# Performance work log

Measured on AMD Instinct MI355X. Metric: run time of the kernel, lower is better.

Reference implementation:

```python
import jax, jax.numpy as jnp
import numpy as np

H, D, H1, L = 4, 128, 512, 2
EPS = 1e-5


def _seg_softmax(logits, seg, n):
    # numerically stable softmax over edges grouped by destination node
    mx = jax.ops.segment_max(logits, seg, num_segments=n)
    mx = jnp.where(jnp.isfinite(mx), mx, 0.0)
    e = jnp.exp(logits - mx[seg])
    s = jax.ops.segment_sum(e, seg, num_segments=n)
    return e / (s[seg] + 1e-16)


def _layernorm(x, g, b):
    mu = x.mean(-1, keepdims=True)
    var = ((x - mu) ** 2).mean(-1, keepdims=True)
    return (x - mu) * jax.lax.rsqrt(var + EPS) * g + b


def _hgt_forward(x_paper, x_author, Wp_paper, bp_paper, Wp_author, bp_author,
                 Wk, bk, Wq, bq, Wv, bv, Wa, ba, skip,
                 a_rel, m_rel, p_rel, ln_g, ln_b,
                 W256, b256, W128, b128,
                 ei_cites, ei_writes, ei_writtenby):
    Np, Na = x_paper.shape[0], x_author.shape[0]
    hp = x_paper @ Wp_paper + bp_paper   # [Np, 512]
    ha = x_author @ Wp_author + bp_author  # [Na, 512]
    scale = 1.0 / jnp.sqrt(jnp.float32(D))

    def kqv(h, l, t):
        k = (h @ Wk[l, t] + bk[l, t]).reshape(-1, H, D)
        q = (h @ Wq[l, t] + bq[l, t]).reshape(-1, H, D)
        v = (h @ Wv[l, t] + bv[l, t]).reshape(-1, H, D)
        return k, q, v

    def rel_msgs(k_src, v_src, q_dst, ei, l, r):
        src, dst = ei[0], ei[1]
        kr = jnp.einsum('nhd,hde->nhe', k_src, a_rel[l, r])  # per-src-node relation transform
        vr = jnp.einsum('nhd,hde->nhe', v_src, m_rel[l, r])
        alpha = (q_dst[dst] * kr[src]).sum(-1) * p_rel[l, r] * scale  # [E, H]
        return alpha, vr[src], dst

    for l in range(L):
        kp, qp, vp = kqv(hp, l, 0)
        ka, qa, va = kqv(ha, l, 1)
        # paper receives: cites (paper->paper, rel 0) + writes (author->paper, rel 1)
        a0, m0, d0 = rel_msgs(kp, vp, qp, ei_cites, l, 0)
        a1, m1, d1 = rel_msgs(ka, va, qp, ei_writes, l, 1)
        al = jnp.concatenate([a0, a1], 0)
        mg = jnp.concatenate([m0, m1], 0)
        ds = jnp.concatenate([d0, d1], 0)
        al = _seg_softmax(al, ds, Np)
        op = jax.ops.segment_sum(al[:, :, None] * mg, ds, num_segments=Np).reshape(Np, H1)
        # author receives: written_by (paper->author, rel 2)
        a2, m2, d2 = rel_msgs(kp, vp, qa, ei_writtenby, l, 2)
        a2 = _seg_softmax(a2, d2, Na)
        oa = jax.ops.segment_sum(a2[:, :, None] * m2, d2, num_segments=Na).reshape(Na, H1)
        # per-dst-type output linear on gelu, then sigmoid-gated skip (HGTConv)
        op = jax.nn.gelu(op, approximate=False) @ Wa[l, 0] + ba[l, 0]
        oa = jax.nn.gelu(oa, approximate=False) @ Wa[l, 1] + ba[l, 1]
        sp = jax.nn.sigmoid(skip[l, 0])
        sa = jax.nn.sigmoid(skip[l, 1])
        op = sp * op + (1.0 - sp) * hp
        oa = sa * oa + (1.0 - sa) * ha
        # encoder wrapper: residual + shared LayerNorm + ReLU (dropout = identity in eval)
        hp = jax.nn.relu(_layernorm(op + hp, ln_g[l], ln_b[l]))
        ha = jax.nn.relu(_layernorm(oa + ha, ln_g[l], ln_b[l]))

    hp = jax.nn.relu(hp @ W256 + b256) @ W128 + b128
    ha = jax.nn.relu(ha @ W256 + b256) @ W128 + b128
    return hp, ha


def setup_inputs() -> dict:
    key = jax.random.key(0)
    ks = iter(jax.random.split(key, 48))
    Np, Na, IN = 30000, 10000, 768
    Ec, Ew, Eb = 150000, 80000, 80000
    f = lambda *s: jax.random.normal(next(ks), s, jnp.float32) * 0.02
    ri = lambda n, e: jax.random.randint(next(ks), (e,), 0, n, jnp.int32)
    inp = {
        'x_paper': jax.random.normal(next(ks), (Np, IN), jnp.float32),
        'x_author': jax.random.normal(next(ks), (Na, IN), jnp.float32),
        'Wp_paper': f(IN, H1), 'bp_paper': jnp.zeros((H1,), jnp.float32),
        'Wp_author': f(IN, H1), 'bp_author': jnp.zeros((H1,), jnp.float32),
        'Wk': f(L, 2, H1, H1), 'bk': jnp.zeros((L, 2, H1), jnp.float32),
        'Wq': f(L, 2, H1, H1), 'bq': jnp.zeros((L, 2, H1), jnp.float32),
        'Wv': f(L, 2, H1, H1), 'bv': jnp.zeros((L, 2, H1), jnp.float32),
        'Wa': f(L, 2, H1, H1), 'ba': jnp.zeros((L, 2, H1), jnp.float32),
        'skip': jnp.ones((L, 2), jnp.float32),
        'a_rel': f(L, 3, H, D, D), 'm_rel': f(L, 3, H, D, D),
        'p_rel': jnp.ones((L, 3, H), jnp.float32),
        'ln_g': jnp.ones((L, H1), jnp.float32), 'ln_b': jnp.zeros((L, H1), jnp.float32),
        'W256': f(H1, 256), 'b256': jnp.zeros((256,), jnp.float32),
        'W128': f(256, 128), 'b128': jnp.zeros((128,), jnp.float32),
        'ei_cites': jnp.stack([ri(Np, Ec), ri(Np, Ec)]),
        'ei_writes': jnp.stack([ri(Na, Ew), ri(Np, Ew)]),
        'ei_writtenby': jnp.stack([ri(Np, Eb), ri(Na, Eb)]),
    }
    return inp


def reference(x_paper, x_author, Wp_paper, bp_paper, Wp_author, bp_author,
              Wk, bk, Wq, bq, Wv, bv, Wa, ba, skip,
              a_rel, m_rel, p_rel, ln_g, ln_b,
              W256, b256, W128, b128,
              ei_cites, ei_writes, ei_writtenby):
    return _hgt_forward(x_paper, x_author, Wp_paper, bp_paper, Wp_author, bp_author,
                        Wk, bk, Wq, bq, Wv, bv, Wa, ba, skip,
                        a_rel, m_rel, p_rel, ln_g, ln_b,
                        W256, b256, W128, b128,
                        ei_cites, ei_writes, ei_writtenby)
```

## Files before the change

### kernel.cpp

```cpp
#include <hip/hip_runtime.h>
#include <hip/hip_bf16.h>
#include <math.h>

#define NHEAD 4
#define DH 128
#define HID 512
#define NLAY 2
#define NP 30000
#define NA 10000
#define INDIM 768
#define EC 150000
#define EW 80000
#define EB 80000
#define NQP 2560
#define NQA 1536

typedef __hip_bfloat16 bf16;
typedef __attribute__((ext_vector_type(8))) short bf16x8;
typedef __attribute__((ext_vector_type(4))) float f32x4;
typedef __attribute__((ext_vector_type(4))) unsigned int u32x4;

__device__ __forceinline__ unsigned short f2bu(float f){ bf16 t = __float2bfloat16(f); return *(unsigned short*)&t; }
__device__ __forceinline__ float bu2f(unsigned short u){ return __uint_as_float((unsigned)u << 16); }

__device__ __forceinline__ void load8b(const bf16* __restrict__ p, int i8, float* o){
  uint4 r = ((const uint4*)p)[i8];
  o[0]=__uint_as_float(r.x<<16); o[1]=__uint_as_float(r.x&0xffff0000u);
  o[2]=__uint_as_float(r.y<<16); o[3]=__uint_as_float(r.y&0xffff0000u);
  o[4]=__uint_as_float(r.z<<16); o[5]=__uint_as_float(r.z&0xffff0000u);
  o[6]=__uint_as_float(r.w<<16); o[7]=__uint_as_float(r.w&0xffff0000u);
}

__device__ __forceinline__ void gload16(const void* g, void* l) {
  __builtin_amdgcn_global_load_lds((const __attribute__((address_space(1))) void*)g,
                                   (__attribute__((address_space(3))) void*)l, 16, 0, 0);
}

struct GemmPair {
  const bf16 *A0, *A1, *B0, *B1;
  const float *b0, *b1;
  void *C0, *C1;
  int lda0, lda1, ldb0, ldb1, ldc0, ldc1;
  int M0, M1, K0, K1;
  int act0, act1, bf0, bf1;
  int nbn0, nbn1, nw0;
};

#define TSTRIDE 132

__global__ __launch_bounds__(256)
void mfma_gemm2(GemmPair gp)
{
  __shared__ __align__(16) short smem[32768];
  const int tid = threadIdx.x;
  const int lane = tid & 63, w = tid >> 6;
  const int nwg = gridDim.x;
  const int bid = blockIdx.x;
  const int xcd = bid & 7, pos = bid >> 3;
  const int q8 = nwg >> 3, r8 = nwg & 7;
  const int work = (xcd < r8 ? xcd * (q8 + 1) : r8 * (q8 + 1) + (xcd - r8) * q8) + pos;
  const int g = work >= gp.nw0;
  const int w2 = g ? work - gp.nw0 : work;
  const bf16* A  = g ? gp.A1 : gp.A0;
  const bf16* Bt = g ? gp.B1 : gp.B0;
  const float* bias = g ? gp.b1 : gp.b0;
  void* Cv = g ? gp.C1 : gp.C0;
  const int lda = g ? gp.lda1 : gp.lda0;
  const int ldb = g ? gp.ldb1 : gp.ldb0;
  const int ldc = g ? gp.ldc1 : gp.ldc0;
  const int M = g ? gp.M1 : gp.M0;
  const int K = g ? gp.K1 : gp.K0;
  const int act = g ? gp.act1 : gp.act0;
  const int isbf = g ? gp.bf1 : gp.bf0;
  const int nbn = g ? gp.nbn1 : gp.nbn0;
  const int brow = (w2 / nbn) * 128, bcol = (w2 % nbn) * 128;
  const int wr = w >> 1, wc = w & 1;

  f32x4 acc[4][4];
#pragma unroll
  for (int m = 0; m < 4; m++)
#pragma unroll
    for (int n = 0; n < 4; n++) acc[m][n] = (f32x4){0.f, 0.f, 0.f, 0.f};

  auto STAGE = [&](int buf, int k0) {
    short* Asb = smem + buf * 8192;
    short* Bsb = smem + 16384 + buf * 8192;
#pragma unroll
    for (int i = 0; i < 4; i++) {
      int chunk = i * 4 + w;
      int c_lin = chunk * 64 + lane;
      int row = c_lin >> 3;
      int kc = ((c_lin & 7) ^ (row & 7)) * 8;
      int growA = brow + row; growA = growA < M ? growA : M - 1;
      gload16(A + (size_t)growA * lda + k0 + kc, Asb + chunk * 512);
      gload16(Bt + (size_t)(bcol + row) * ldb + k0 + kc, Bsb + chunk * 512);
    }
  };

  const int nk = K >> 6;
  STAGE(0, 0);
  __syncthreads();
  int buf = 0;
  for (int t = 0; t < nk; t++) {
    if (t + 1 < nk) STAGE(buf ^ 1, (t + 1) << 6);
    const short* Asb = smem + buf * 8192;
    const short* Bsb = smem + 16384 + buf * 8192;
#pragma unroll
    for (int kk = 0; kk < 2; kk++) {
      const int ke = kk * 32 + (lane >> 4) * 8;
      bf16x8 af[4], bq[4];
#pragma unroll
      for (int m = 0; m < 4; m++) {
        int row = wr * 64 + m * 16 + (lane & 15);
        af[m] = *(const bf16x8*)(Asb + row * 64 + (ke ^ ((row & 7) << 3)));
      }
#pragma unroll
      for (int n = 0; n < 4; n++) {
        int col = wc * 64 + n * 16 + (lane & 15);
        bq[n] = *(const bf16x8*)(Bsb + col * 64 + (ke ^ ((col & 7) << 3)));
      }
#pragma unroll
      for (int m = 0; m < 4; m++)
#pragma unroll
        for (int n = 0; n < 4; n++)
          acc[m][n] = __builtin_amdgcn_mfma_f32_16x16x32_bf16(af[m], bq[n], acc[m][n], 0, 0, 0);
    }
    __syncthreads();
    buf ^= 1;
  }

  if (isbf) {
#pragma unroll
    for (int m = 0; m < 4; m++) {
      int row0 = wr * 64 + m * 16 + (lane >> 4) * 4;
#pragma unroll
      for (int n = 0; n < 4; n++) {
        int col = wc * 64 + n * 16 + (lane & 15);
        float bv = bias ? bias[bcol + col] : 0.f;
#pragma unroll
        for (int r = 0; r < 4; r++) {
          float v = acc[m][n][r] + bv;
          if (act) v = fmaxf(v, 0.f);
          smem[(row0 + r) * TSTRIDE + col] = (short)f2bu(v);
        }
      }
    }
    __syncthreads();
#pragma unroll
    for (int it = 0; it < 8; it++) {
      int chunk = it * 256 + tid;
      int row = chunk >> 4, c16 = chunk & 15;
      int gr = brow + row;
      if (gr < M) {
        u32x4 v = *(const u32x4*)(smem + row * TSTRIDE + c16 * 8);
        __builtin_nontemporal_store(v,
            (u32x4*)((unsigned short*)Cv + (size_t)gr * ldc + bcol + c16 * 8));
      }
    }
  } else {
#pragma unroll
    for (int m = 0; m < 4; m++) {
      int gr0 = brow + wr * 64 + m * 16 + (lane >> 4) * 4;
#pragma unroll
      for (int n = 0; n < 4; n++) {
        int gc = bcol + wc * 64 + n * 16 + (lane & 15);
        float bv = bias ? bias[gc] : 0.f;
#pragma unroll
        for (int r = 0; r < 4; r++) {
          int gr = gr0 + r;
          if (gr < M) {
            float v = acc[m][n][r] + bv;
            if (act) v = fmaxf(v, 0.f);
            __builtin_nontemporal_store(v, (float*)Cv + (size_t)gr * ldc + gc);
          }
        }
      }
    }
  }
}

struct FuseArgs {
  const float* W[12];
  const float* rel[12];
  const float* bin[12];
  float* out[12];
  float* bout[12];
};
struct TrArgs {
  const float* src[20];
  bf16* dst[20];
};
struct CopyB { const float* src[4]; float* dst[4]; };

__global__ __launch_bounds__(256)
void gemm_fuse(FuseArgs fa)
{
  int c = blockIdx.z >> 2, h = blockIdx.z & 3;
  const float* A = fa.W[c] + h * 128;
  const float* B = fa.rel[c] + (size_t)h * 128 * 128;
  float* C = fa.out[c] + h * 128;
  __shared__ float Ast[64][17];
  __shared__ float Bst[16][64];
  const int tid = threadIdx.x;
  const int tx = tid & 15, ty = tid >> 4;
  const int bm = blockIdx.x * 64, bn = blockIdx.y * 64;
  float acc[4][4] = {};
  for (int k0 = 0; k0 < 128; k0 += 16) {
#pragma unroll
    for (int i = 0; i < 4; i++) {
      int lin = tid + i * 256;
      int m = lin >> 4, kk = lin & 15;
      Ast[m][kk] = A[(size_t)(bm + m) * 512 + k0 + kk];
      int kb = lin >> 6, nb = lin & 63;
      Bst[kb][nb] = B[(size_t)(k0 + kb) * 128 + bn + nb];
    }
    __syncthreads();
#pragma unroll
    for (int kk = 0; kk < 16; kk++) {
      float a[4], b[4];
#pragma unroll
      for (int i = 0; i < 4; i++) a[i] = Ast[ty * 4 + i][kk];
#pragma unroll
      for (int j = 0; j < 4; j++) b[j] = Bst[kk][tx * 4 + j];
#pragma unroll
      for (int i = 0; i < 4; i++)
#pragma unroll
        for (int j = 0; j < 4; j++)
          acc[i][j] = fmaf(a[i], b[j], acc[i][j]);
    }
    __syncthreads();
  }
#pragma unroll
  for (int i = 0; i < 4; i++)
#pragma unroll
    for (int j = 0; j < 4; j++)
      C[(size_t)(bm + ty * 4 + i) * 512 + bn + tx * 4 + j] = acc[i][j];
}

__global__ __launch_bounds__(256)
void transpose20(TrArgs ta)
{
  int c = blockIdx.z;
  const float* in = ta.src[c];
  bf16* o = ta.dst[c];
  __shared__ float t[32][33];
  int bn = blockIdx.x * 32, bk = blockIdx.y * 32;
  int x = threadIdx.x, y = threadIdx.y;
#pragma unroll
  for (int i = 0; i < 32; i += 8)
    t[y + i][x] = in[(size_t)(bk + y + i) * 512 + bn + x];
  __syncthreads();
#pragma unroll
  for (int i = 0; i < 32; i += 8)
    o[(size_t)(bn + y + i) * 512 + bk + x] = __float2bfloat16(t[x][y + i]);
}

__global__ __launch_bounds__(512)
void bias_fuse_all(FuseArgs fa)
{
  int c = blockIdx.x;
  int j = threadIdx.x;
  int h = j >> 7, e = j & 127;
  const float* bh = fa.bin[c] + h * DH;
  const float* rh = fa.rel[c] + (size_t)h * DH * DH;
  float s = 0.f;
  for (int d = 0; d < DH; d++) s = fmaf(bh[d], rh[d * DH + e], s);
  fa.bout[c][j] = s;
}

__global__ __launch_bounds__(512)
void copy_bias(CopyB cb)
{
  cb.dst[blockIdx.x][threadIdx.x] = cb.src[blockIdx.x][threadIdx.x];
}

__global__ __launch_bounds__(256)
void transpose_to_bf16(const float* __restrict__ in, bf16* __restrict__ out,
                       int K_, int N_)
{
  __shared__ float t[32][33];
  int bn = blockIdx.x * 32, bk = blockIdx.y * 32;
  int x = threadIdx.x, y = threadIdx.y;
#pragma unroll
  for (int i = 0; i < 32; i += 8) {
    int k = bk + y + i, n = bn + x;
    if (k < K_ && n < N_) t[y + i][x] = in[(size_t)k * N_ + n];
  }
  __syncthreads();
#pragma unroll
  for (int i = 0; i < 32; i += 8) {
    int n = bn + y + i, k = bk + x;
    if (n < N_ && k < K_) out[(size_t)n * K_ + k] = __float2bfloat16(t[x][y + i]);
  }
}

__global__ __launch_bounds__(256)
void f32_to_bf16_2(const float* __restrict__ s0, bf16* __restrict__ d0, long long n0,
                   const float* __restrict__ s1, bf16* __restrict__ d1, long long n1)
{
  long long i = ((long long)blockIdx.x * 256 + threadIdx.x) * 4;
  const float* s; bf16* d;
  if (i < n0) { s = s0; d = d0; }
  else { i -= n0; if (i >= n1) return; s = s1; d = d1; }
  float4 v = *(const float4*)(s + i);
  ushort4 o;
  o.x = f2bu(v.x); o.y = f2bu(v.y); o.z = f2bu(v.z); o.w = f2bu(v.w);
  *(ushort4*)(d + i) = o;
}

__global__ __launch_bounds__(256)
void build_hist(const int* __restrict__ ei_dst, int E, int* __restrict__ deg)
{
  int i = blockIdx.x * 256 + threadIdx.x;
  if (i < E) atomicAdd(&deg[ei_dst[i]], 1);
}

__global__ __launch_bounds__(256)
void scan_blk(const int* __restrict__ deg, int n, int* __restrict__ rowptr,
              int* __restrict__ bsum)
{
  __shared__ int sh[256];
  int t = threadIdx.x;
  int base = blockIdx.x * 1024 + t * 4;
  int v0 = 0, v1 = 0, v2 = 0, v3 = 0;
  if (base + 3 < n) {
    int4 v = *(const int4*)(deg + base);
    v0 = v.x; v1 = v.y; v2 = v.z; v3 = v.w;
  } else {
    if (base < n)     v0 = deg[base];
    if (base + 1 < n) v1 = deg[base + 1];
    if (base + 2 < n) v2 = deg[base + 2];
    if (base + 3 < n) v3 = deg[base + 3];
  }
  int s = v0 + v1 + v2 + v3;
  sh[t] = s;
  __syncthreads();
#pragma unroll
  for (int off = 1; off < 256; off <<= 1) {
    int tv = (t >= off) ? sh[t - off] : 0;
    __syncthreads();
    sh[t] += tv;
    __syncthreads();
  }
  int excl = sh[t] - s;
  if (t == 255) bsum[blockIdx.x] = sh[255];
  if (base < n)     rowptr[base] = excl;
  if (base + 1 < n) rowptr[base + 1] = excl + v0;
  if (base + 2 < n) rowptr[base + 2] = excl + v0 + v1;
  if (base + 3 < n) rowptr[base + 3] = excl + v0 + v1 + v2;
}

__global__ __launch_bounds__(64)
void scan_bsum(int* __restrict__ bsum, int nb, int* __restrict__ rowptr_end)
{
  int t = threadIdx.x;
  int v = (t < nb) ? bsum[t] : 0;
  int inc = v;
#pragma unroll
  for (int off = 1; off < 64; off <<= 1) {
    int o = __shfl_up(inc, off);
    if (t >= off) inc += o;
  }
  if (t < nb) bsum[t] = inc - v;
  if (t == nb - 1) *rowptr_end = inc;
}

__global__ __launch_bounds__(256)
void scan_add(int* __restrict__ rowptr, const int* __restrict__ bsum, int n)
{
  int add = bsum[blockIdx.x];
  if (add == 0) return;
  int i = blockIdx.x * 1024 + threadIdx.x * 4;
  if (i < n)     rowptr[i] += add;
  if (i + 1 < n) rowptr[i + 1] += add;
  if (i + 2 < n) rowptr[i + 2] += add;
  if (i + 3 < n) rowptr[i + 3] += add;
}

__global__ __launch_bounds__(256)
void build_scatter(const int* __restrict__ ei, int E, int flag,
                   const int* __restrict__ rowptr, int* __restrict__ cursor,
                   int* __restrict__ srcs)
{
  int e = blockIdx.x * 256 + threadIdx.x;
  if (e >= E) return;
  int src = ei[e];
  int dst = ei[E + e];
  int pos = rowptr[dst] + atomicAdd(&cursor[dst], 1);
  srcs[pos] = src | flag;
}

__global__ __launch_bounds__(256)
void csr_attn_agg2(const int* __restrict__ rowptrP, const int* __restrict__ srcsP,
                   const int* __restrict__ rowptrA, const int* __restrict__ srcsA,
                   const bf16* __restrict__ qkvP, const bf16* __restrict__ qkvA,
                   const float* __restrict__ prl, float scale,
                   bf16* __restrict__ agP, bf16* __restrict__ agA)
{
  int node = blockIdx.x * 4 + (threadIdx.x >> 6);
  int lane = threadIdx.x & 63;
  int h = lane >> 4;
  const int* rp; const int* srcs;
  const bf16* q; const bf16 *t0, *t1;
  int ld0, off0, ld1, off1;
  float p0, p1;
  bf16* outp;
  if (node < NP) {
    rp = rowptrP; srcs = srcsP;
    q = qkvP + (size_t)node * NQP;
    t0 = qkvP; ld0 = NQP; off0 = 512;
    t1 = qkvA; ld1 = NQA; off1 = 512;
    p0 = prl[h] * scale; p1 = prl[4 + h] * scale;
    outp = agP + (size_t)node * HID;
  } else {
    int r = node - NP;
    if (r >= NA) return;
    rp = rowptrA; srcs = srcsA; node = r;
    q = qkvA + (size_t)r * NQA;
    t0 = qkvP; ld0 = NQP; off0 = 1536;
    t1 = qkvP; ld1 = NQP; off1 = 1536;
    p0 = prl[8 + h] * scale; p1 = p0;
    outp = agA + (size_t)r * HID;
  }
  float qv[8];
  load8b(q, lane, qv);
  int beg = rp[node], end = rp[node + 1];
  float m = -INFINITY, s = 0.f;
  float acc[8] = {};
  for (int p = beg; p < end; ++p) {
    int se = srcs[p];
    int src = se & 0x3FFFFFFF;
    bool f1 = (se & 0x40000000) != 0;
    const bf16* row = f1 ? (t1 + (size_t)src * ld1 + off1)
                         : (t0 + (size_t)src * ld0 + off0);
    float kv[8], vv[8];
    load8b(row, lane, kv);
    load8b(row + 512, lane, vv);
    float a = 0.f;
#pragma unroll
    for (int i = 0; i < 8; i++) a = fmaf(qv[i], kv[i], a);
    a += __shfl_xor(a, 1);
    a += __shfl_xor(a, 2);
    a += __shfl_xor(a, 4);
    a += __shfl_xor(a, 8);
    a *= f1 ? p1 : p0;
    if (a > m + 8.f) {
      float sc = __expf(m - a);
      s *= sc;
#pragma unroll
      for (int i = 0; i < 8; i++) acc[i] *= sc;
      m = a;
    }
    float wgt = __expf(a - m);
    s += wgt;
#pragma unroll
    for (int i = 0; i < 8; i++) acc[i] = fmaf(wgt, vv[i], acc[i]);
  }
  float inv = 1.f / (s + 1e-16f);
  unsigned short gg[8];
#pragma unroll
  for (int i = 0; i < 8; i++) {
    float v = acc[i] * inv;
    gg[i] = f2bu(0.5f * v * (1.f + erff(v * 0.70710678118654752f)));
  }
  uint4 o;
  o.x = gg[0] | ((unsigned)gg[1] << 16);
  o.y = gg[2] | ((unsigned)gg[3] << 16);
  o.z = gg[4] | ((unsigned)gg[5] << 16);
  o.w = gg[6] | ((unsigned)gg[7] << 16);
  *(uint4*)(outp + lane * 8) = o;
}

__global__ __launch_bounds__(256)
void skip_ln_relu2(const bf16* __restrict__ oplP, const bf16* __restrict__ oplA,
                   bf16* __restrict__ hP, bf16* __restrict__ hA,
                   const float* __restrict__ skip2,
                   const float* __restrict__ g, const float* __restrict__ b)
{
  int row = blockIdx.x;
  const bf16* orow; bf16* hrow; float sk;
  if (row < NP) {
    orow = oplP + (size_t)row * HID; hrow = hP + (size_t)row * HID; sk = skip2[0];
  } else {
    int r = row - NP;
    orow = oplA + (size_t)r * HID; hrow = hA + (size_t)r * HID; sk = skip2[1];
  }
  float sp = 1.f / (1.f + expf(-sk));
  int t = threadIdx.x;
  ushort2 ov = ((const ushort2*)orow)[t];
  ushort2 hv = ((ushort2*)hrow)[t];
  float t0 = sp * bu2f(ov.x) + (2.f - sp) * bu2f(hv.x);
  float t1 = sp * bu2f(ov.y) + (2.f - sp) * bu2f(hv.y);
  float s = t0 + t1, ss = t0 * t0 + t1 * t1;
#pragma unroll
  for (int off = 32; off; off >>= 1) {
    s += __shfl_down(s, off);
    ss += __shfl_down(ss, off);
  }
  __shared__ float sh[8];
  int wid = t >> 6, lane = t & 63;
  if (lane == 0) { sh[wid] = s; sh[4 + wid] = ss; }
  __syncthreads();
  if (t == 0) {
    float S = 0, SS = 0;
    for (int wv = 0; wv < 4; wv++) { S += sh[wv]; SS += sh[4 + wv]; }
    sh[0] = S; sh[4] = SS;
  }
  __syncthreads();
  float mu = sh[0] * (1.f / 512.f);
  float var = sh[4] * (1.f / 512.f) - mu * mu;
  float inv = rsqrtf(var + 1e-5f);
  float y0 = (t0 - mu) * inv * g[2 * t] + b[2 * t];
  float y1 = (t1 - mu) * inv * g[2 * t + 1] + b[2 * t + 1];
  ushort2 o;
  o.x = f2bu(fmaxf(y0, 0.f));
  o.y = f2bu(fmaxf(y1, 0.f));
  ((ushort2*)hrow)[t] = o;
}

static inline void mgemm2(GemmPair gp, int N0, int N1, hipStream_t s)
{
  gp.nbn0 = N0 / 128;
  gp.nbn1 = N1 / 128;
  int nw0 = ((gp.M0 + 127) / 128) * gp.nbn0;
  int nw1 = ((gp.M1 + 127) / 128) * gp.nbn1;
  gp.nw0 = nw0;
  mfma_gemm2<<<dim3(nw0 + nw1), 256, 0, s>>>(gp);
}

extern "C" void kernel_launch(void* const* d_in, const int* in_sizes, int n_in,
                              void* d_out, int out_size, void* d_ws, size_t ws_size,
                              hipStream_t stream)
{
  const float* x_paper  = (const float*)d_in[0];
  const float* x_author = (const float*)d_in[1];
  const float* Wp_paper = (const float*)d_in[2];
  const float* bp_paper = (const float*)d_in[3];
  const float* Wp_author= (const float*)d_in[4];
  const float* bp_author= (const float*)d_in[5];
  const float* Wk = (const float*)d_in[6];
  const float* bk = (const float*)d_in[7];
  const float* Wq = (const float*)d_in[8];
  const float* bq = (const float*)d_in[9];
  const float* Wv = (const float*)d_in[10];
  const float* bv = (const float*)d_in[11];
  const float* Wa = (const float*)d_in[12];
  const float* ba = (const float*)d_in[13];
  const float* skip = (const float*)d_in[14];
  const float* a_rel = (const float*)d_in[15];
  const float* m_rel = (const float*)d_in[16];
  const float* p_rel = (const float*)d_in[17];
  const float* ln_g = (const float*)d_in[18];
  const float* ln_b = (const float*)d_in[19];
  const float* W256 = (const float*)d_in[20];
  const float* b256 = (const float*)d_in[21];
  const float* W128 = (const float*)d_in[22];
  const float* b128 = (const float*)d_in[23];
  const int* ei_c = (const int*)d_in[24];
  const int* ei_w = (const int*)d_in[25];
  const int* ei_b = (const int*)d_in[26];
  float* out = (float*)d_out;

  const size_t NPe = (size_t)NP * HID, NAe = (size_t)NA * HID;
  const size_t HH = (size_t)HID * HID;
  char* w = (char*)d_ws;
  size_t off = 0;
  auto alloc = [&](size_t bytes) -> void* {
    void* p = (void*)(w + off);
    off += (bytes + 255) & ~(size_t)255;
    return p;
  };
  bf16* hb_p  = (bf16*)alloc(NPe * 2);
  bf16* hb_a  = (bf16*)alloc(NAe * 2);
  bf16* qkv_p = (bf16*)alloc((size_t)NP * NQP * 2);
  bf16* qkv_a = (bf16*)alloc((size_t)NA * NQA * 2);
  bf16* ag_p  = (bf16*)alloc(NPe * 2);
  bf16* ag_a  = (bf16*)alloc(NAe * 2);
  float* Wf32 = (float*)alloc(12 * HH * 4);
  bf16* WBtP  = (bf16*)alloc((size_t)2 * NQP * HID * 2);
  bf16* WBtA  = (bf16*)alloc((size_t)2 * NQA * HID * 2);
  float* pbP  = (float*)alloc((size_t)2 * NQP * 4);
  float* pbA  = (float*)alloc((size_t)2 * NQA * 4);
  bf16* WaT   = (bf16*)alloc(4 * HH * 2);
  bf16* W256T = (bf16*)alloc((size_t)HID * 256 * 2);
  bf16* W128T = (bf16*)alloc((size_t)256 * 128 * 2);
  bf16* WpTp  = (bf16*)alloc((size_t)INDIM * HID * 2);
  bf16* WpTa  = (bf16*)alloc((size_t)INDIM * HID * 2);
  int* rowptrP = (int*)alloc((size_t)(NP + 1) * 4);
  int* degP    = (int*)alloc((size_t)NP * 4);
  int* srcsP   = (int*)alloc((size_t)(EC + EW) * 4);
  int* rowptrA = (int*)alloc((size_t)(NA + 1) * 4);
  int* degA    = (int*)alloc((size_t)NA * 4);
  int* srcsA   = (int*)alloc((size_t)EB * 4);
  int* bsumP   = (int*)alloc(64 * 4);
  int* bsumA   = (int*)alloc(64 * 4);
  if (off > ws_size) return;

  const float scale = 0.08838834764831845f;
  const int nbP = (NP + 1023) / 1024, nbA = (NA + 1023) / 1024;

  (void)hipMemsetAsync(degP, 0, (size_t)NP * 4, stream);
  (void)hipMemsetAsync(degA, 0, (size_t)NA * 4, stream);
  build_hist<<<dim3((EC + 255) / 256), 256, 0, stream>>>(ei_c + EC, EC, degP);
  build_hist<<<dim3((EW + 255) / 256), 256, 0, stream>>>(ei_w + EW, EW, degP);
  build_hist<<<dim3((EB + 255) / 256), 256, 0, stream>>>(ei_b + EB, EB, degA);
  scan_blk<<<dim3(nbP), 256, 0, stream>>>(degP, NP, rowptrP, bsumP);
  scan_bsum<<<dim3(1), 64, 0, stream>>>(bsumP, nbP, rowptrP + NP);
  scan_add<<<dim3(nbP), 256, 0, stream>>>(rowptrP, bsumP, NP);
  scan_blk<<<dim3(nbA), 256, 0, stream>>>(degA, NA, rowptrA, bsumA);
  scan_bsum<<<dim3(1), 64, 0, stream>>>(bsumA, nbA, rowptrA + NA);
  scan_add<<<dim3(nbA), 256, 0, stream>>>(rowptrA, bsumA, NA);
  (void)hipMemsetAsync(degP, 0, (size_t)NP * 4, stream);
  (void)hipMemsetAsync(degA, 0, (size_t)NA * 4, stream);
  build_scatter<<<dim3((EC + 255) / 256), 256, 0, stream>>>(ei_c, EC, 0,
      rowptrP, degP, srcsP);
  build_scatter<<<dim3((EW + 255) / 256), 256, 0, stream>>>(ei_w, EW, 0x40000000,
      rowptrP, degP, srcsP);
  build_scatter<<<dim3((EB + 255) / 256), 256, 0, stream>>>(ei_b, EB, 0,
      rowptrA, degA, srcsA);

  FuseArgs fa;
  TrArgs ta;
  CopyB cb;
  for (int l = 0; l < NLAY; l++) {
    bf16* packP = WBtP + (size_t)l * NQP * HID;
    bf16* packA = WBtA + (size_t)l * NQA * HID;
    float* pbPl = pbP + (size_t)l * NQP;
    float* pbAl = pbA + (size_t)l * NQA;
    for (int r = 0; r < 3; r++)
      for (int s = 0; s < 2; s++) {
        int c = (l * 3 + r) * 2 + s;
        int t = (r == 1) ? 1 : 0;
        fa.W[c]   = (s == 0 ? Wk : Wv) + (size_t)(l * 2 + t) * HH;
        fa.rel[c] = (s == 0 ? a_rel : m_rel) + (size_t)(l * 3 + r) * NHEAD * DH * DH;
        fa.bin[c] = (s == 0 ? bk : bv) + (size_t)(l * 2 + t) * HID;
        fa.out[c] = Wf32 + (size_t)c * HH;
        ta.src[c] = fa.out[c];
        if (r == 0) {
          ta.dst[c]  = packP + (size_t)(512 + s * 512) * HID;
          fa.bout[c] = pbPl + 512 + s * 512;
        } else if (r == 1) {
          ta.dst[c]  = packA + (size_t)(512 + s * 512) * HID;
          fa.bout[c] = pbAl + 512 + s * 512;
        } else {
          ta.dst[c]  = packP + (size_t)(1536 + s * 512) * HID;
          fa.bout[c] = pbPl + 1536 + s * 512;
        }
      }
    ta.src[12 + l * 2 + 0] = Wq + (size_t)(l * 2 + 0) * HH;
    ta.dst[12 + l * 2 + 0] = packP;
    ta.src[12 + l * 2 + 1] = Wq + (size_t)(l * 2 + 1) * HH;
    ta.dst[12 + l * 2 + 1] = packA;
    ta.src[16 + l * 2 + 0] = Wa + (size_t)(l * 2 + 0) * HH;
    ta.dst[16 + l * 2 + 0] = WaT + (size_t)(l * 2 + 0) * HH;
    ta.src[16 + l * 2 + 1] = Wa + (size_t)(l * 2 + 1) * HH;
    ta.dst[16 + l * 2 + 1] = WaT + (size_t)(l * 2 + 1) * HH;
    cb.src[l * 2 + 0] = bq + (size_t)(l * 2 + 0) * HID;
    cb.dst[l * 2 + 0] = pbPl;
    cb.src[l * 2 + 1] = bq + (size_t)(l * 2 + 1) * HID;
    cb.dst[l * 2 + 1] = pbAl;
  }
  gemm_fuse<<<dim3(8, 2, 48), 256, 0, stream>>>(fa);
  transpose20<<<dim3(16, 16, 20), dim3(32, 8), 0, stream>>>(ta);
  bias_fuse_all<<<dim3(12), 512, 0, stream>>>(fa);
  copy_bias<<<dim3(4), 512, 0, stream>>>(cb);
  {
    dim3 b(32, 8);
    transpose_to_bf16<<<dim3(8, 16), b, 0, stream>>>(W256, W256T, HID, 256);
    transpose_to_bf16<<<dim3(4, 8), b, 0, stream>>>(W128, W128T, 256, 128);
    transpose_to_bf16<<<dim3(16, 24), b, 0, stream>>>(Wp_paper, WpTp, INDIM, HID);
    transpose_to_bf16<<<dim3(16, 24), b, 0, stream>>>(Wp_author, WpTa, INDIM, HID);
  }

  bf16* xb_p = qkv_p;
  bf16* xb_a = qkv_a;
  long long nxp = (long long)NP * INDIM, nxa = (long long)NA * INDIM;
  f32_to_bf16_2<<<dim3((int)(((nxp + nxa) / 4 + 255) / 256)), 256, 0, stream>>>(
      x_paper, xb_p, nxp, x_author, xb_a, nxa);
  {
    GemmPair gp{};
    gp.A0 = xb_p; gp.lda0 = INDIM; gp.B0 = WpTp; gp.ldb0 = INDIM;
    gp.b0 = bp_paper; gp.C0 = hb_p; gp.ldc0 = HID;
    gp.M0 = NP; gp.K0 = INDIM; gp.act0 = 0; gp.bf0 = 1;
    gp.A1 = xb_a; gp.lda1 = INDIM; gp.B1 = WpTa; gp.ldb1 = INDIM;
    gp.b1 = bp_author; gp.C1 = hb_a; gp.ldc1 = HID;
    gp.M1 = NA; gp.K1 = INDIM; gp.act1 = 0; gp.bf1 = 1;
    mgemm2(gp, HID, HID, stream);
  }

  for (int l = 0; l < NLAY; l++) {
    const float* prl = p_rel + (size_t)l * 3 * NHEAD;
    const bf16* packP = WBtP + (size_t)l * NQP * HID;
    const bf16* packA = WBtA + (size_t)l * NQA * HID;
    const float* pbPl = pbP + (size_t)l * NQP;
    const float* pbAl = pbA + (size_t)l * NQA;

    {
      GemmPair gp{};
      gp.A0 = hb_p; gp.lda0 = HID; gp.B0 = packP; gp.ldb0 = HID;
      gp.b0 = pbPl; gp.C0 = qkv_p; gp.ldc0 = NQP;
      gp.M0 = NP; gp.K0 = HID; gp.act0 = 0; gp.bf0 = 1;
      gp.A1 = hb_a; gp.lda1 = HID; gp.B1 = packA; gp.ldb1 = HID;
      gp.b1 = pbAl; gp.C1 = qkv_a; gp.ldc1 = NQA;
      gp.M1 = NA; gp.K1 = HID; gp.act1 = 0; gp.bf1 = 1;
      mgemm2(gp, NQP, NQA, stream);
    }
    csr_attn_agg2<<<dim3((NP + NA + 3) / 4), 256, 0, stream>>>(
        rowptrP, srcsP, rowptrA, srcsA, qkv_p, qkv_a, prl, scale, ag_p, ag_a);
    bf16* opl_p = qkv_p;
    bf16* opl_a = qkv_a;
    {
      GemmPair gp{};
      gp.A0 = ag_p; gp.lda0 = HID; gp.B0 = WaT + (size_t)(l * 2 + 0) * HH; gp.ldb0 = HID;
      gp.b0 = ba + (size_t)(l * 2 + 0) * HID; gp.C0 = opl_p; gp.ldc0 = HID;
      gp.M0 = NP; gp.K0 = HID; gp.act0 = 0; gp.bf0 = 1;
      gp.A1 = ag_a; gp.lda1 = HID; gp.B1 = WaT + (size_t)(l * 2 + 1) * HH; gp.ldb1 = HID;
      gp.b1 = ba + (size_t)(l * 2 + 1) * HID; gp.C1 = opl_a; gp.ldc1 = HID;
      gp.M1 = NA; gp.K1 = HID; gp.act1 = 0; gp.bf1 = 1;
      mgemm2(gp, HID, HID, stream);
    }
    skip_ln_relu2<<<dim3(NP + NA), 256, 0, stream>>>(
        opl_p, opl_a, hb_p, hb_a, skip + l * 2,
        ln_g + (size_t)l * HID, ln_b + (size_t)l * HID);
  }

  bf16* h256_p = ag_p;
  bf16* h256_a = ag_a;
  {
    GemmPair gp{};
    gp.A0 = hb_p; gp.lda0 = HID; gp.B0 = W256T; gp.ldb0 = HID;
    gp.b0 = b256; gp.C0 = h256_p; gp.ldc0 = 256;
    gp.M0 = NP; gp.K0 = HID; gp.act0 = 1; gp.bf0 = 1;
    gp.A1 = hb_a; gp.lda1 = HID; gp.B1 = W256T; gp.ldb1 = HID;
    gp.b1 = b256; gp.C1 = h256_a; gp.ldc1 = 256;
    gp.M1 = NA; gp.K1 = HID; gp.act1 = 1; gp.bf1 = 1;
    mgemm2(gp, 256, 256, stream);
  }
  {
    GemmPair gp{};
    gp.A0 = h256_p; gp.lda0 = 256; gp.B0 = W128T; gp.ldb0 = 256;
    gp.b0 = b128; gp.C0 = out; gp.ldc0 = 128;
    gp.M0 = NP; gp.K0 = 256; gp.act0 = 0; gp.bf0 = 0;
    gp.A1 = h256_a; gp.lda1 = 256; gp.B1 = W128T; gp.ldb1 = 256;
    gp.b1 = b128; gp.C1 = out + (size_t)NP * 128; gp.ldc1 = 128;
    gp.M1 = NA; gp.K1 = 256; gp.act1 = 0; gp.bf1 = 0;
    mgemm2(gp, 128, 128, stream);
  }
}
```

Baseline: 898.1 us.

## Add 256x256-tile 512-thread MFMA GEMM and merge CSR build kernels

Adds a new bf16 MFMA GEMM kernel with 256x256 output tiles, 8 waves of 128x64 each and double-buffered, XOR-swizzled LDS staging. All bf16-output GEMMs use it; the final fp32-output projection keeps the old kernel. The larger tile raises arithmetic intensity and cuts global operand traffic per output. In exchange the kernel uses 128KB of LDS and 128 accumulator floats per thread, so occupancy and spill risk go up, and coarser tiles mean fewer workgroups on small GEMMs. Separately, the per-relation histogram, scan and scatter kernels for CSR construction are merged into single launches with one memset, to cut launch overhead.

```diff
diff --git a/kernel.cpp b/kernel.cpp
--- a/kernel.cpp
+++ b/kernel.cpp
@@ -45,6 +45,121 @@
   int act0, act1, bf0, bf1;
   int nbn0, nbn1, nw0;
 };
+
+#define TS3 260
+
+__global__ __launch_bounds__(512, 2)
+void mfma_gemm3(GemmPair gp)
+{
+  __shared__ __align__(16) short smem[65536];
+  const int tid = threadIdx.x;
+  const int lane = tid & 63, w = tid >> 6;
+  const int nwg = gridDim.x;
+  const int bid = blockIdx.x;
+  const int xcd = bid & 7, pos = bid >> 3;
+  const int q8 = nwg >> 3, r8 = nwg & 7;
+  const int work = (xcd < r8 ? xcd * (q8 + 1) : r8 * (q8 + 1) + (xcd - r8) * q8) + pos;
+  const int g = work >= gp.nw0;
+  const int w2 = g ? work - gp.nw0 : work;
+  const bf16* A  = g ? gp.A1 : gp.A0;
+  const bf16* Bt = g ? gp.B1 : gp.B0;
+  const float* bias = g ? gp.b1 : gp.b0;
+  void* Cv = g ? gp.C1 : gp.C0;
+  const int lda = g ? gp.lda1 : gp.lda0;
+  const int ldb = g ? gp.ldb1 : gp.ldb0;
+  const int ldc = g ? gp.ldc1 : gp.ldc0;
+  const int M = g ? gp.M1 : gp.M0;
+  const int K = g ? gp.K1 : gp.K0;
+  const int act = g ? gp.act1 : gp.act0;
+  const int nbn = g ? gp.nbn1 : gp.nbn0;
+  const int brow = (w2 / nbn) * 256, bcol = (w2 % nbn) * 256;
+  const int wr = w >> 2, wc = w & 3;
+
+  f32x4 acc[8][4];
+#pragma unroll
+  for (int m = 0; m < 8; m++)
+#pragma unroll
+    for (int n = 0; n < 4; n++) acc[m][n] = (f32x4){0.f, 0.f, 0.f, 0.f};
+
+  auto STAGE = [&](int buf, int k0) {
+    short* Asb = smem + buf * 16384;
+    short* Bsb = smem + 32768 + buf * 16384;
+#pragma unroll
+    for (int i = 0; i < 4; i++) {
+      int cw = i * 8 + w;
+      int c_lin = cw * 64 + lane;
+      int row = c_lin >> 3;
+      int kc = ((c_lin & 7) ^ (row & 7)) * 8;
+      int growA = brow + row; growA = growA < M ? growA : M - 1;
+      gload16(A + (size_t)growA * lda + k0 + kc, Asb + cw * 512);
+      gload16(Bt + (size_t)(bcol + row) * ldb + k0 + kc, Bsb + cw * 512);
+    }
+  };
+
+  const int nk = K >> 6;
+  STAGE(0, 0);
+  __syncthreads();
+  int buf = 0;
+  for (int t = 0; t < nk; t++) {
+    if (t + 1 < nk) STAGE(buf ^ 1, (t + 1) << 6);
+    const short* Asb = smem + buf * 16384;
+    const short* Bsb = smem + 32768 + buf * 16384;
+#pragma unroll
+    for (int kk = 0; kk < 2; kk++) {
+      const int ke = kk * 32 + (lane >> 4) * 8;
+      bf16x8 bq[4];
+#pragma unroll
+      for (int n = 0; n < 4; n++) {
+        int col = wc * 64 + n * 16 + (lane & 15);
+        bq[n] = *(const bf16x8*)(Bsb + col * 64 + (ke ^ ((col & 7) << 3)));
+      }
+#pragma unroll
+      for (int m = 0; m < 8; m++) {
+        int row = wr * 128 + m * 16 + (lane & 15);
+        bf16x8 af = *(const bf16x8*)(Asb + row * 64 + (ke ^ ((row & 7) << 3)));
+#pragma unroll
+        for (int n = 0; n < 4; n++)
+          acc[m][n] = __builtin_amdgcn_mfma_f32_16x16x32_bf16(af, bq[n], acc[m][n], 0, 0, 0);
+      }
+    }
+    __syncthreads();
+    buf ^= 1;
+  }
+
+#pragma unroll
+  for (int half = 0; half < 2; half++) {
+    __syncthreads();
+    if (wr == half) {
+#pragma unroll
+      for (int m = 0; m < 8; m++) {
+        int rl0 = m * 16 + (lane >> 4) * 4;
+#pragma unroll
+        for (int n = 0; n < 4; n++) {
+          int col = wc * 64 + n * 16 + (lane & 15);
+          float bv = bias ? bias[bcol + col] : 0.f;
+#pragma unroll
+          for (int r = 0; r < 4; r++) {
+            float v = acc[m][n][r] + bv;
+            if (act) v = fmaxf(v, 0.f);
+            smem[(rl0 + r) * TS3 + col] = (short)f2bu(v);
+          }
+        }
+      }
+    }
+    __syncthreads();
+#pragma unroll
+    for (int it = 0; it < 8; it++) {
+      int chunk = it * 512 + tid;
+      int row = chunk >> 5, c16 = chunk & 31;
+      int gr = brow + half * 128 + row;
+      if (gr < M) {
+        u32x4 v = *(const u32x4*)(smem + row * TS3 + c16 * 8);
+        __builtin_nontemporal_store(v,
+            (u32x4*)((unsigned short*)Cv + (size_t)gr * ldc + bcol + c16 * 8));
+      }
+    }
+  }
+}
 
 #define TSTRIDE 132
 
@@ -309,19 +424,23 @@
 }
 
 __global__ __launch_bounds__(256)
-void build_hist(const int* __restrict__ ei_dst, int E, int* __restrict__ deg)
+void build_hist3(const int* __restrict__ eiC, const int* __restrict__ eiW,
+                 const int* __restrict__ eiB,
+                 int* __restrict__ degP, int* __restrict__ degA)
 {
   int i = blockIdx.x * 256 + threadIdx.x;
-  if (i < E) atomicAdd(&deg[ei_dst[i]], 1);
-}
-
-__global__ __launch_bounds__(256)
-void scan_blk(const int* __restrict__ deg, int n, int* __restrict__ rowptr,
-              int* __restrict__ bsum)
+  if (i < EC) atomicAdd(&degP[eiC[EC + i]], 1);
+  else if (i < EC + EW) atomicAdd(&degP[eiW[EW + (i - EC)]], 1);
+  else if (i < EC + EW + EB) atomicAdd(&degA[eiB[EB + (i - EC - EW)]], 1);
+}
+
+__device__ __forceinline__ void scan_blk_body(const int* __restrict__ deg, int n,
+                                              int* __restrict__ rowptr,
+                                              int* __restrict__ bsum, int blk)
 {
   __shared__ int sh[256];
   int t = threadIdx.x;
-  int base = blockIdx.x * 1024 + t * 4;
+  int base = blk * 1024 + t * 4;
   int v0 = 0, v1 = 0, v2 = 0, v3 = 0;
   if (base + 3 < n) {
     int4 v = *(const int4*)(deg + base);
@@ -343,16 +462,31 @@
     __syncthreads();
   }
   int excl = sh[t] - s;
-  if (t == 255) bsum[blockIdx.x] = sh[255];
+  if (t == 255) bsum[blk] = sh[255];
   if (base < n)     rowptr[base] = excl;
   if (base + 1 < n) rowptr[base + 1] = excl + v0;
   if (base + 2 < n) rowptr[base + 2] = excl + v0 + v1;
   if (base + 3 < n) rowptr[base + 3] = excl + v0 + v1 + v2;
 }
 
+#define NBP ((NP + 1023) / 1024)
+#define NBA ((NA + 1023) / 1024)
+
+__global__ __launch_bounds__(256)
+void scan_blk2(const int* __restrict__ degP, int* __restrict__ rowptrP, int* __restrict__ bsumP,
+               const int* __restrict__ degA, int* __restrict__ rowptrA, int* __restrict__ bsumA)
+{
+  if (blockIdx.x < NBP) scan_blk_body(degP, NP, rowptrP, bsumP, blockIdx.x);
+  else                  scan_blk_body(degA, NA, rowptrA, bsumA, blockIdx.x - NBP);
+}
+
 __global__ __launch_bounds__(64)
-void scan_bsum(int* __restrict__ bsum, int nb, int* __restrict__ rowptr_end)
-{
+void scan_bsum2(int* __restrict__ bsumP, int* __restrict__ endP,
+                int* __restrict__ bsumA, int* __restrict__ endA)
+{
+  int* bsum = blockIdx.x ? bsumA : bsumP;
+  int nb = blockIdx.x ? NBA : NBP;
+  int* rpe = blockIdx.x ? endA : endP;
   int t = threadIdx.x;
   int v = (t < nb) ? bsum[t] : 0;
   int inc = v;
@@ -362,15 +496,19 @@
     if (t >= off) inc += o;
   }
   if (t < nb) bsum[t] = inc - v;
-  if (t == nb - 1) *rowptr_end = inc;
-}
-
-__global__ __launch_bounds__(256)
-void scan_add(int* __restrict__ rowptr, const int* __restrict__ bsum, int n)
-{
-  int add = bsum[blockIdx.x];
+  if (t == nb - 1) *rpe = inc;
+}
+
+__global__ __launch_bounds__(256)
+void scan_add2(int* __restrict__ rowptrP, const int* __restrict__ bsumP,
+               int* __restrict__ rowptrA, const int* __restrict__ bsumA)
+{
+  int* rowptr; const int* bsum; int n, blk;
+  if (blockIdx.x < NBP) { rowptr = rowptrP; bsum = bsumP; n = NP; blk = blockIdx.x; }
+  else                  { rowptr = rowptrA; bsum = bsumA; n = NA; blk = blockIdx.x - NBP; }
+  int add = bsum[blk];
   if (add == 0) return;
-  int i = blockIdx.x * 1024 + threadIdx.x * 4;
+  int i = blk * 1024 + threadIdx.x * 4;
   if (i < n)     rowptr[i] += add;
   if (i + 1 < n) rowptr[i + 1] += add;
   if (i + 2 < n) rowptr[i + 2] += add;
@@ -378,16 +516,29 @@
 }
 
 __global__ __launch_bounds__(256)
-void build_scatter(const int* __restrict__ ei, int E, int flag,
-                   const int* __restrict__ rowptr, int* __restrict__ cursor,
-                   int* __restrict__ srcs)
-{
-  int e = blockIdx.x * 256 + threadIdx.x;
-  if (e >= E) return;
-  int src = ei[e];
-  int dst = ei[E + e];
-  int pos = rowptr[dst] + atomicAdd(&cursor[dst], 1);
-  srcs[pos] = src | flag;
+void build_scatter3(const int* __restrict__ eiC, const int* __restrict__ eiW,
+                    const int* __restrict__ eiB,
+                    const int* __restrict__ rowptrP, int* __restrict__ curP,
+                    int* __restrict__ srcsP,
+                    const int* __restrict__ rowptrA, int* __restrict__ curA,
+                    int* __restrict__ srcsA)
+{
+  int i = blockIdx.x * 256 + threadIdx.x;
+  if (i < EC) {
+    int src = eiC[i], dst = eiC[EC + i];
+    int pos = rowptrP[dst] + atomicAdd(&curP[dst], 1);
+    srcsP[pos] = src;
+  } else if (i < EC + EW) {
+    int e = i - EC;
+    int src = eiW[e], dst = eiW[EW + e];
+    int pos = rowptrP[dst] + atomicAdd(&curP[dst], 1);
+    srcsP[pos] = src | 0x40000000;
+  } else if (i < EC + EW + EB) {
+    int e = i - EC - EW;
+    int src = eiB[e], dst = eiB[EB + e];
+    int pos = rowptrA[dst] + atomicAdd(&curA[dst], 1);
+    srcsA[pos] = src;
+  }
 }
 
 __global__ __launch_bounds__(256)
@@ -526,6 +677,16 @@
   int nw1 = ((gp.M1 + 127) / 128) * gp.nbn1;
   gp.nw0 = nw0;
   mfma_gemm2<<<dim3(nw0 + nw1), 256, 0, s>>>(gp);
+}
+
+static inline void mgemm3(GemmPair gp, int N0, int N1, hipStream_t s)
+{
+  gp.nbn0 = N0 / 256;
+  gp.nbn1 = N1 / 256;
+  int nw0 = ((gp.M0 + 255) / 256) * gp.nbn0;
+  int nw1 = ((gp.M1 + 255) / 256) * gp.nbn1;
+  gp.nw0 = nw0;
+  mfma_gemm3<<<dim3(nw0 + nw1), 512, 0, s>>>(gp);
 }
 
 extern "C" void kernel_launch(void* const* d_in, const int* in_sizes, int n_in,
@@ -587,37 +748,26 @@
   bf16* WpTp  = (bf16*)alloc((size_t)INDIM * HID * 2);
   bf16* WpTa  = (bf16*)alloc((size_t)INDIM * HID * 2);
   int* rowptrP = (int*)alloc((size_t)(NP + 1) * 4);
-  int* degP    = (int*)alloc((size_t)NP * 4);
+  int* rowptrA = (int*)alloc((size_t)(NA + 1) * 4);
+  int* degP    = (int*)alloc((size_t)(2 * NP + 2 * NA) * 4);
+  int* degA    = degP + NP;
+  int* curP    = degA + NA;
+  int* curA    = curP + NP;
   int* srcsP   = (int*)alloc((size_t)(EC + EW) * 4);
-  int* rowptrA = (int*)alloc((size_t)(NA + 1) * 4);
-  int* degA    = (int*)alloc((size_t)NA * 4);
   int* srcsA   = (int*)alloc((size_t)EB * 4);
   int* bsumP   = (int*)alloc(64 * 4);
   int* bsumA   = (int*)alloc(64 * 4);
   if (off > ws_size) return;
 
   const float scale = 0.08838834764831845f;
-  const int nbP = (NP + 1023) / 1024, nbA = (NA + 1023) / 1024;
-
-  (void)hipMemsetAsync(degP, 0, (size_t)NP * 4, stream);
-  (void)hipMemsetAsync(degA, 0, (size_t)NA * 4, stream);
-  build_hist<<<dim3((EC + 255) / 256), 256, 0, stream>>>(ei_c + EC, EC, degP);
-  build_hist<<<dim3((EW + 255) / 256), 256, 0, stream>>>(ei_w + EW, EW, degP);
-  build_hist<<<dim3((EB + 255) / 256), 256, 0, stream>>>(ei_b + EB, EB, degA);
-  scan_blk<<<dim3(nbP), 256, 0, stream>>>(degP, NP, rowptrP, bsumP);
-  scan_bsum<<<dim3(1), 64, 0, stream>>>(bsumP, nbP, rowptrP + NP);
-  scan_add<<<dim3(nbP), 256, 0, stream>>>(rowptrP, bsumP, NP);
-  scan_blk<<<dim3(nbA), 256, 0, stream>>>(degA, NA, rowptrA, bsumA);
-  scan_bsum<<<dim3(1), 64, 0, stream>>>(bsumA, nbA, rowptrA + NA);
-  scan_add<<<dim3(nbA), 256, 0, stream>>>(rowptrA, bsumA, NA);
-  (void)hipMemsetAsync(degP, 0, (size_t)NP * 4, stream);
-  (void)hipMemsetAsync(degA, 0, (size_t)NA * 4, stream);
-  build_scatter<<<dim3((EC + 255) / 256), 256, 0, stream>>>(ei_c, EC, 0,
-      rowptrP, degP, srcsP);
-  build_scatter<<<dim3((EW + 255) / 256), 256, 0, stream>>>(ei_w, EW, 0x40000000,
-      rowptrP, degP, srcsP);
-  build_scatter<<<dim3((EB + 255) / 256), 256, 0, stream>>>(ei_b, EB, 0,
-      rowptrA, degA, srcsA);
+
+  (void)hipMemsetAsync(degP, 0, (size_t)(2 * NP + 2 * NA) * 4, stream);
+  build_hist3<<<dim3((EC + EW + EB + 255) / 256), 256, 0, stream>>>(ei_c, ei_w, ei_b, degP, degA);
+  scan_blk2<<<dim3(NBP + NBA), 256, 0, stream>>>(degP, rowptrP, bsumP, degA, rowptrA, bsumA);
+  scan_bsum2<<<dim3(2), 64, 0, stream>>>(bsumP, rowptrP + NP, bsumA, rowptrA + NA);
+  scan_add2<<<dim3(NBP + NBA), 256, 0, stream>>>(rowptrP, bsumP, rowptrA, bsumA);
+  build_scatter3<<<dim3((EC + EW + EB + 255) / 256), 256, 0, stream>>>(
+      ei_c, ei_w, ei_b, rowptrP, curP, srcsP, rowptrA, curA, srcsA);
 
   FuseArgs fa;
   TrArgs ta;
@@ -685,7 +835,7 @@
     gp.A1 = xb_a; gp.lda1 = INDIM; gp.B1 = WpTa; gp.ldb1 = INDIM;
     gp.b1 = bp_author; gp.C1 = hb_a; gp.ldc1 = HID;
     gp.M1 = NA; gp.K1 = INDIM; gp.act1 = 0; gp.bf1 = 1;
-    mgemm2(gp, HID, HID, stream);
+    mgemm3(gp, HID, HID, stream);
   }
 
   for (int l = 0; l < NLAY; l++) {
@@ -703,7 +853,7 @@
       gp.A1 = hb_a; gp.lda1 = HID; gp.B1 = packA; gp.ldb1 = HID;
       gp.b1 = pbAl; gp.C1 = qkv_a; gp.ldc1 = NQA;
       gp.M1 = NA; gp.K1 = HID; gp.act1 = 0; gp.bf1 = 1;
-      mgemm2(gp, NQP, NQA, stream);
+      mgemm3(gp, NQP, NQA, stream);
     }
     csr_attn_agg2<<<dim3((NP + NA + 3) / 4), 256, 0, stream>>>(
         rowptrP, srcsP, rowptrA, srcsA, qkv_p, qkv_a, prl, scale, ag_p, ag_a);
@@ -717,7 +867,7 @@
       gp.A1 = ag_a; gp.lda1 = HID; gp.B1 = WaT + (size_t)(l * 2 + 1) * HH; gp.ldb1 = HID;
       gp.b1 = ba + (size_t)(l * 2 + 1) * HID; gp.C1 = opl_a; gp.ldc1 = HID;
       gp.M1 = NA; gp.K1 = HID; gp.act1 = 0; gp.bf1 = 1;
-      mgemm2(gp, HID, HID, stream);
+      mgemm3(gp, HID, HID, stream);
     }
     skip_ln_relu2<<<dim3(NP + NA), 256, 0, stream>>>(
         opl_p, opl_a, hb_p, hb_a, skip + l * 2,
@@ -734,7 +884,7 @@
     gp.A1 = hb_a; gp.lda1 = HID; gp.B1 = W256T; gp.ldb1 = HID;
     gp.b1 = b256; gp.C1 = h256_a; gp.ldc1 = 256;
     gp.M1 = NA; gp.K1 = HID; gp.act1 = 1; gp.bf1 = 1;
-    mgemm2(gp, 256, 256, stream);
+    mgemm3(gp, 256, 256, stream);
   }
   {
     GemmPair gp{};
```

Measured after the change: 918.3 us. 2.2% more time.
